# Kernel tuning notes

Hardware: AMD Instinct MI355X
Metric: run time of the kernel (lower is better)

Reference implementation:

```python
import jax, jax.numpy as jnp
import numpy as np

K_F = 3          # propagation kernel
PAD_F = 1
NUM = K_F * K_F - 1   # 8 non-reference neighbors
IDX_REF = NUM // 2    # 4
PROP_TIME = 18
B, H, W = 4, 240, 1216


def _conv2d_same(x, w, b):
    # x: (B,Cin,H,W), w: (Cout,Cin,kh,kw)
    y = jax.lax.conv_general_dilated(x, w, (1, 1), 'SAME',
                                     dimension_numbers=('NCHW', 'OIHW', 'NCHW'))
    return y + b[None, :, None, None]


def _bilinear(img, y, x):
    # img: (B,H,W); y,x: (B,K,H,W) float sample coords. Zero outside bounds (DCN semantics).
    Bv, Hv, Wv = img.shape
    flat = img.reshape(Bv, -1)
    y0 = jnp.floor(y)
    x0 = jnp.floor(x)
    wy = y - y0
    wx = x - x0

    def g(yy, xx):
        valid = (yy >= 0) & (yy <= Hv - 1) & (xx >= 0) & (xx <= Wv - 1)
        yc = jnp.clip(yy, 0, Hv - 1).astype(jnp.int32)
        xc = jnp.clip(xx, 0, Wv - 1).astype(jnp.int32)
        idx = (yc * Wv + xc).reshape(Bv, -1)
        v = jnp.take_along_axis(flat, idx, axis=1).reshape(yy.shape)
        return jnp.where(valid, v, jnp.zeros((), img.dtype))

    return ((1 - wy) * (1 - wx) * g(y0, x0)
            + (1 - wy) * wx * g(y0, x0 + 1)
            + wy * (1 - wx) * g(y1 := y0 + 1, x0)
            + wy * wx * g(y1, x0 + 1))


def _deform_agg(feat, off, mask, k, pad):
    # Modulated deformable conv with w == 1, b == 0, ch_f == 1.
    # feat: (B,1,H,W); off: (B,K,2,H,W) (dy,dx); mask: (B,K,H,W)
    Bv, _, Hv, Wv = feat.shape
    kk = jnp.arange(k)
    by = (jnp.repeat(kk, k) - pad).astype(feat.dtype)  # kernel base dy, row-major
    bx = (jnp.tile(kk, k) - pad).astype(feat.dtype)    # kernel base dx
    gy = jnp.arange(Hv, dtype=feat.dtype)[None, None, :, None]
    gx = jnp.arange(Wv, dtype=feat.dtype)[None, None, None, :]
    y = gy + by[None, :, None, None] + off[:, :, 0]
    x = gx + bx[None, :, None, None] + off[:, :, 1]
    s = _bilinear(feat[:, 0], y, x)                    # (B,K,H,W)
    return jnp.sum(s * mask, axis=1, keepdims=True)


def setup_inputs() -> dict:
    key = jax.random.key(0)
    k1, k2, k3, k4, k5, k6 = jax.random.split(key, 6)
    feat_init = jax.random.uniform(k1, (B, 1, H, W), jnp.float32)
    guidance = jax.random.normal(k2, (B, 8, H, W), jnp.float32)
    confidence = jax.random.uniform(k3, (B, 1, H, W), jnp.float32)
    dep = jax.random.uniform(k4, (B, 1, H, W), jnp.float32)
    valid = (jax.random.uniform(k5, (B, 1, H, W), jnp.float32) < 0.05)
    feat_fix = dep * valid.astype(jnp.float32)
    w_oa = 0.1 * jax.random.normal(k6, (3 * NUM, 8, 3, 3), jnp.float32)
    b_oa = jnp.zeros((3 * NUM,), jnp.float32)
    aff_scale_const = jnp.full((1,), 0.5 * NUM, jnp.float32)  # gamma * num (TGASS)
    return {'feat_init': feat_init, 'guidance': guidance, 'confidence': confidence,
            'feat_fix': feat_fix, 'w_oa': w_oa, 'b_oa': b_oa,
            'aff_scale_const': aff_scale_const}


def reference(feat_init, guidance, confidence, feat_fix, w_oa, b_oa, aff_scale_const):
    Bv, _, Hv, Wv = guidance.shape
    oa = _conv2d_same(guidance, w_oa, b_oa)                 # (B,24,H,W)
    o1, o2, aff = oa[:, :NUM], oa[:, NUM:2 * NUM], oa[:, 2 * NUM:]
    # torch: cat((o1,o2),1).view(B,num,2,H,W) then insert zero ref offset at idx_ref
    off = jnp.concatenate([o1, o2], axis=1).reshape(Bv, NUM, 2, Hv, Wv)
    zeros = jnp.zeros((Bv, 1, 2, Hv, Wv), off.dtype)
    off = jnp.concatenate([off[:, :IDX_REF], zeros, off[:, IDX_REF:]], axis=1)  # (B,9,2,H,W)

    # TGASS affinity
    aff = jnp.tanh(aff) / (aff_scale_const + 1e-8)          # (B,8,H,W)

    # confidence-weighted affinity: 1x1 deform-sample of confidence at each neighbor offset
    nbr = jnp.array([0, 1, 2, 3, 5, 6, 7, 8])
    off_c = jax.lax.stop_gradient(off[:, nbr])              # (B,8,2,H,W), offsets detached
    gy = jnp.arange(Hv, dtype=aff.dtype)[None, None, :, None]
    gx = jnp.arange(Wv, dtype=aff.dtype)[None, None, None, :]
    conf_aff = _bilinear(confidence[:, 0], gy + off_c[:, :, 0], gx + off_c[:, :, 1])
    aff = aff * conf_aff

    s = jnp.sum(jnp.abs(aff), axis=1, keepdims=True) + 1e-4
    s = jnp.maximum(s, 1.0)                                 # TGASS clamp
    aff = aff / s
    aff_ref = 1.0 - jnp.sum(aff, axis=1, keepdims=True)
    aff9 = jnp.concatenate([aff[:, :IDX_REF], aff_ref, aff[:, IDX_REF:]], axis=1)  # (B,9,H,W)

    # preserve_input mask
    mask_fix = (jnp.sum((feat_fix > 0.0).astype(feat_fix.dtype), axis=1, keepdims=True) > 0.0)
    mask_fix = jax.lax.stop_gradient(mask_fix.astype(feat_fix.dtype))

    def step(feat, _):
        feat = (1.0 - mask_fix) * feat + mask_fix * feat_fix
        feat = _deform_agg(feat, off, aff9, K_F, PAD_F)
        return feat, None

    feat_result, _ = jax.lax.scan(step, feat_init, None, length=PROP_TIME)
    return feat_result, off.reshape(Bv, -1, Hv, Wv), aff9
```

## Files before the change

### kernel.cpp

```cpp
#include <hip/hip_runtime.h>
#include <hip/hip_bf16.h>

#define B_ 4
#define H_ 240
#define W_ 1216
#define HW_ (H_*W_)
#define N1_ (B_*HW_)
#define PT_ 18

#define TROWS 11
#define TCOLS 274

__device__ __forceinline__ bool probe_bf16(const void* scale_ptr) {
    return ((const unsigned short*)scale_ptr)[0] == 0x4080;
}

__device__ __forceinline__ float ldin(const void* p, int i, bool bf) {
    if (bf) {
        unsigned int u = (unsigned int)((const unsigned short*)p)[i];
        return __uint_as_float(u << 16);
    }
    return ((const float*)p)[i];
}

__device__ __forceinline__ void stout(void* p, int i, bool bf, float v) {
    if (bf) ((__hip_bfloat16*)p)[i] = __float2bfloat16(v);
    else    ((float*)p)[i] = v;
}

__global__ __launch_bounds__(256) void k_prep_w(const void* __restrict__ w_oa,
                                                const void* __restrict__ b_oa,
                                                const void* __restrict__ scale,
                                                float* __restrict__ wc) {
    bool bf = probe_bf16(scale);
    int i = blockIdx.x * 256 + threadIdx.x;
    if (i < 1728) wc[i] = ldin(w_oa, i, bf);
    if (i < 24)   wc[1728 + i] = ldin(b_oa, i, bf);
}

__global__ __launch_bounds__(256) void k_init(const void* __restrict__ finit,
                                              const void* __restrict__ ffix,
                                              const void* __restrict__ scale,
                                              float* __restrict__ featA) {
    bool bf = probe_bf16(scale);
    int p = blockIdx.x * 256 + threadIdx.x;
    if (p >= N1_) return;
    float fx = ldin(ffix, p, bf);
    featA[p] = (fx > 0.0f) ? fx : ldin(finit, p, bf);
}

__global__ __launch_bounds__(256) void k_conv(const void* __restrict__ guid,
                                              const void* __restrict__ conf,
                                              const void* __restrict__ scale,
                                              const float* __restrict__ wc,
                                              void* __restrict__ d_out,
                                              float* __restrict__ ws_off,
                                              float* __restrict__ ws_aff,
                                              int mode2) {
    bool bf = probe_bf16(scale);
    int p = blockIdx.x * 256 + threadIdx.x;
    if (p >= N1_) return;
    int b = p / HW_;
    int r = p - b * HW_;
    int h = r / W_;
    int w = r - h * W_;

    float g[8][9];
    #pragma unroll
    for (int t = 0; t < 9; ++t) {
        int hh = h + t / 3 - 1;
        int ww = w + t % 3 - 1;
        bool v = (hh >= 0) && (hh < H_) && (ww >= 0) && (ww < W_);
        int idx0 = hh * W_ + ww;
        #pragma unroll
        for (int ci = 0; ci < 8; ++ci)
            g[ci][t] = v ? ldin(guid, (b * 8 + ci) * HW_ + idx0, bf) : 0.0f;
    }

    float oa[24];
    #pragma unroll
    for (int co = 0; co < 24; ++co) {
        float a = wc[1728 + co];
        #pragma unroll
        for (int ci = 0; ci < 8; ++ci)
            #pragma unroll
            for (int t = 0; t < 9; ++t)
                a = fmaf(g[ci][t], wc[(co * 8 + ci) * 9 + t], a);
        oa[co] = a;
    }

    float scl = ldin(scale, 0, bf);
    float inv = 1.0f / (scl + 1e-8f);

    float aft[8];
    int cbase = b * HW_;
    #pragma unroll
    for (int t = 0; t < 8; ++t) {
        float a = tanhf(oa[16 + t]) * inv;
        float y = (float)h + oa[2 * t];
        float x = (float)w + oa[2 * t + 1];
        float y0f = floorf(y), x0f = floorf(x);
        int y0 = (int)y0f, x0 = (int)x0f;
        float wy = y - y0f, wx = x - x0f;
        int y0c = min(max(y0, 0), H_ - 1), y1c = min(max(y0 + 1, 0), H_ - 1);
        int x0c = min(max(x0, 0), W_ - 1), x1c = min(max(x0 + 1, 0), W_ - 1);
        bool vy0 = (y0 >= 0) && (y0 < H_), vy1 = (y0 >= -1) && (y0 < H_ - 1);
        bool vx0 = (x0 >= 0) && (x0 < W_), vx1 = (x0 >= -1) && (x0 < W_ - 1);
        float w00 = (1.0f - wy) * (1.0f - wx); w00 = (vy0 && vx0) ? w00 : 0.0f;
        float w01 = (1.0f - wy) * wx;          w01 = (vy0 && vx1) ? w01 : 0.0f;
        float w10 = wy * (1.0f - wx);          w10 = (vy1 && vx0) ? w10 : 0.0f;
        float w11 = wy * wx;                   w11 = (vy1 && vx1) ? w11 : 0.0f;
        float f00 = ldin(conf, cbase + y0c * W_ + x0c, bf);
        float f01 = ldin(conf, cbase + y0c * W_ + x1c, bf);
        float f10 = ldin(conf, cbase + y1c * W_ + x0c, bf);
        float f11 = ldin(conf, cbase + y1c * W_ + x1c, bf);
        float cv = w00 * f00 + w01 * f01 + w10 * f10 + w11 * f11;
        aft[t] = a * cv;
    }
    float s = 1e-4f;
    #pragma unroll
    for (int t = 0; t < 8; ++t) s += fabsf(aft[t]);
    s = fmaxf(s, 1.0f);
    float rs = 1.0f / s;
    float suma = 0.0f;
    #pragma unroll
    for (int t = 0; t < 8; ++t) { aft[t] *= rs; suma += aft[t]; }
    float aref = 1.0f - suma;

    #pragma unroll
    for (int t = 0; t < 8; ++t) {
        int n9 = t + (t >= 4 ? 1 : 0);
        stout(d_out, N1_ + (b * 18 + 2 * n9)     * HW_ + r, bf, oa[2 * t]);
        stout(d_out, N1_ + (b * 18 + 2 * n9 + 1) * HW_ + r, bf, oa[2 * t + 1]);
        stout(d_out, 19 * N1_ + (b * 9 + n9) * HW_ + r, bf, aft[t]);
    }
    stout(d_out, N1_ + (b * 18 + 8) * HW_ + r, bf, 0.0f);
    stout(d_out, N1_ + (b * 18 + 9) * HW_ + r, bf, 0.0f);
    stout(d_out, 19 * N1_ + (b * 9 + 4) * HW_ + r, bf, aref);

    if (mode2) {
        #pragma unroll
        for (int t = 0; t < 8; ++t) {
            ws_off[t * N1_ + p]       = oa[2 * t];
            ws_off[(8 + t) * N1_ + p] = oa[2 * t + 1];
            int n9 = t + (t >= 4 ? 1 : 0);
            ws_aff[n9 * N1_ + p] = aft[t];
        }
        ws_aff[4 * N1_ + p] = aref;
    }
}

__global__ __launch_bounds__(256) void k_prop(const float* __restrict__ src,
                                              float* __restrict__ dst,
                                              const float* __restrict__ ws_off,
                                              const float* __restrict__ ws_aff,
                                              const void* __restrict__ d_out_all,
                                              const void* __restrict__ ffix_in,
                                              const void* __restrict__ scale,
                                              void* __restrict__ d_out_feat,
                                              int last, int mode2) {
    __shared__ float tile[TROWS][TCOLS];

    int tx = threadIdx.x;
    int bx = blockIdx.x;
    int h  = blockIdx.y;
    int b  = blockIdx.z;
    int w  = bx * 256 + tx;
    bool active = (w < W_);

    const float* sp = src + b * HW_;
    int row0 = h - 5;
    int col0 = bx * 256 - 8;

    bool bf = probe_bf16(scale);
    int r = h * W_ + w;
    int p = b * HW_ + r;
    float oy[8], ox[8], af[9], fxv = 0.0f;
    if (active) {
        if (mode2) {
            #pragma unroll
            for (int t = 0; t < 8; ++t) {
                oy[t] = ws_off[t * N1_ + p];
                ox[t] = ws_off[(8 + t) * N1_ + p];
            }
            #pragma unroll
            for (int n = 0; n < 9; ++n) af[n] = ws_aff[n * N1_ + p];
        } else {
            #pragma unroll
            for (int t = 0; t < 8; ++t) {
                int n9 = t + (t >= 4 ? 1 : 0);
                oy[t] = ldin(d_out_all, N1_ + (b * 18 + 2 * n9)     * HW_ + r, bf);
                ox[t] = ldin(d_out_all, N1_ + (b * 18 + 2 * n9 + 1) * HW_ + r, bf);
            }
            #pragma unroll
            for (int n = 0; n < 9; ++n)
                af[n] = ldin(d_out_all, 19 * N1_ + (b * 9 + n) * HW_ + r, bf);
        }
        if (!last) fxv = ldin(ffix_in, p, bf);
    }

    for (int idx = tx; idx < TROWS * TCOLS; idx += 256) {
        int rr = idx / TCOLS;
        int cc = idx - rr * TCOLS;
        int gy = min(max(row0 + rr, 0), H_ - 1);
        int gx = min(max(col0 + cc, 0), W_ - 1);
        tile[rr][cc] = sp[gy * W_ + gx];
    }
    __syncthreads();
    if (!active) return;

    float acc = af[4] * tile[5][tx + 8];

    #pragma unroll
    for (int t = 0; t < 8; ++t) {
        int n9 = t + (t >= 4 ? 1 : 0);
        float y = (float)(h + n9 / 3 - 1) + oy[t];
        float x = (float)(w + n9 % 3 - 1) + ox[t];
        float y0f = floorf(y), x0f = floorf(x);
        int y0 = (int)y0f, x0 = (int)x0f;
        float wy = y - y0f, wx = x - x0f;
        int y0c = min(max(y0, 0), H_ - 1), y1c = min(max(y0 + 1, 0), H_ - 1);
        int x0c = min(max(x0, 0), W_ - 1), x1c = min(max(x0 + 1, 0), W_ - 1);
        bool vy0 = (y0 >= 0) && (y0 < H_), vy1 = (y0 >= -1) && (y0 < H_ - 1);
        bool vx0 = (x0 >= 0) && (x0 < W_), vx1 = (x0 >= -1) && (x0 < W_ - 1);
        float w00 = (1.0f - wy) * (1.0f - wx); w00 = (vy0 && vx0) ? w00 : 0.0f;
        float w01 = (1.0f - wy) * wx;          w01 = (vy0 && vx1) ? w01 : 0.0f;
        float w10 = wy * (1.0f - wx);          w10 = (vy1 && vx0) ? w10 : 0.0f;
        float w11 = wy * wx;                   w11 = (vy1 && vx1) ? w11 : 0.0f;

        int sy0 = y0c - row0, sy1 = y1c - row0;
        int sx0 = x0c - col0, sx1 = x1c - col0;
        float f00, f01, f10, f11;
        if ((sy0 >= 0) && (sy1 <= TROWS - 1) && (sx0 >= 0) && (sx1 <= TCOLS - 1)) {
            f00 = tile[sy0][sx0];
            f01 = tile[sy0][sx1];
            f10 = tile[sy1][sx0];
            f11 = tile[sy1][sx1];
        } else {
            f00 = sp[y0c * W_ + x0c];
            f01 = sp[y0c * W_ + x1c];
            f10 = sp[y1c * W_ + x0c];
            f11 = sp[y1c * W_ + x1c];
        }
        float v = w00 * f00 + w01 * f01 + w10 * f10 + w11 * f11;
        acc = fmaf(af[n9], v, acc);
    }

    if (last) {
        stout(d_out_feat, p, bf, acc);
    } else {
        dst[p] = (fxv > 0.0f) ? fxv : acc;
    }
}

extern "C" void kernel_launch(void* const* d_in, const int* in_sizes, int n_in,
                              void* d_out, int out_size, void* d_ws, size_t ws_size,
                              hipStream_t stream) {
    const void* feat_init  = d_in[0];
    const void* guidance   = d_in[1];
    const void* confidence = d_in[2];
    const void* feat_fix   = d_in[3];
    const void* w_oa       = d_in[4];
    const void* b_oa       = d_in[5];
    const void* scale      = d_in[6];

    float* wsf    = (float*)d_ws;
    float* featA  = wsf;
    float* featB  = wsf + N1_;
    float* wc     = wsf + 2 * (size_t)N1_;
    float* ws_off = wsf + 2 * (size_t)N1_ + 2048;
    float* ws_aff = ws_off + 16 * (size_t)N1_;

    int is_bf16 = (in_sizes[4] < 1728 * 4) ? 1 : 0;
    size_t need2 = ((size_t)27 * N1_ + 2048) * sizeof(float);
    int mode2 = (is_bf16 && ws_size >= need2) ? 1 : 0;

    int grid = (N1_ + 255) / 256;
    hipLaunchKernelGGL(k_prep_w, dim3(7), dim3(256), 0, stream, w_oa, b_oa, scale, wc);
    hipLaunchKernelGGL(k_init, dim3(grid), dim3(256), 0, stream,
                       feat_init, feat_fix, scale, featA);
    hipLaunchKernelGGL(k_conv, dim3(grid), dim3(256), 0, stream,
                       guidance, confidence, scale, wc, d_out, ws_off, ws_aff, mode2);

    float* a = featA;
    float* bbuf = featB;
    dim3 pgrid(5, H_, B_);
    for (int it = 0; it < PT_; ++it) {
        int last = (it == PT_ - 1) ? 1 : 0;
        hipLaunchKernelGGL(k_prop, pgrid, dim3(256), 0, stream,
                           a, bbuf, ws_off, ws_aff, d_out, feat_fix, scale,
                           d_out, last, mode2);
        float* t = a; a = bbuf; bbuf = t;
    }
}
```

Before: 1.088 ms.

## Tile conv inputs in shared memory and process multiple rows per prop block

The conv kernel now runs on a 2D row-tiled grid. It stages the 3-row guidance window and a confidence tile in LDS, and reads transposed weights so each guidance value is broadcast across all 24 output channels. The propagation kernel handles four rows per block, which shares one taller feature tile and cuts halo reloads and launch block count. The mode2 gating is moved from a host check to a device-side bf16 probe. The trade-offs are more LDS per block and possibly lower occupancy.

Measured after the change: 1.711 ms. 1.57x slower.

```diff
diff --git a/kernel.cpp b/kernel.cpp
--- a/kernel.cpp
+++ b/kernel.cpp
@@ -11,6 +11,12 @@
 #define TROWS 11
 #define TCOLS 274
 
+#define PR_ 4
+#define TROWS2 (PR_ + 10)
+
+#define GCOLS 258
+#define GPITCH 260
+
 __device__ __forceinline__ bool probe_bf16(const void* scale_ptr) {
     return ((const unsigned short*)scale_ptr)[0] == 0x4080;
 }
@@ -34,8 +40,14 @@
                                                 float* __restrict__ wc) {
     bool bf = probe_bf16(scale);
     int i = blockIdx.x * 256 + threadIdx.x;
-    if (i < 1728) wc[i] = ldin(w_oa, i, bf);
-    if (i < 24)   wc[1728 + i] = ldin(b_oa, i, bf);
+    if (i < 1728) {
+        float v = ldin(w_oa, i, bf);
+        wc[i] = v;
+        int co = i / 72;
+        int rem = i - co * 72;
+        wc[1752 + rem * 24 + co] = v;
+    }
+    if (i < 24) wc[1728 + i] = ldin(b_oa, i, bf);
 }
 
 __global__ __launch_bounds__(256) void k_init(const void* __restrict__ finit,
@@ -57,43 +69,65 @@
                                               float* __restrict__ ws_off,
                                               float* __restrict__ ws_aff,
                                               int mode2) {
+    __shared__ float gt[8][3][GPITCH];
+    __shared__ float ct[TROWS][TCOLS];
+
+    int tx = threadIdx.x;
+    int bx = blockIdx.x;
+    int h  = blockIdx.y;
+    int b  = blockIdx.z;
+    int w  = bx * 256 + tx;
+    bool active = (w < W_);
     bool bf = probe_bf16(scale);
-    int p = blockIdx.x * 256 + threadIdx.x;
-    if (p >= N1_) return;
-    int b = p / HW_;
-    int r = p - b * HW_;
-    int h = r / W_;
-    int w = r - h * W_;
-
-    float g[8][9];
-    #pragma unroll
-    for (int t = 0; t < 9; ++t) {
-        int hh = h + t / 3 - 1;
-        int ww = w + t % 3 - 1;
-        bool v = (hh >= 0) && (hh < H_) && (ww >= 0) && (ww < W_);
-        int idx0 = hh * W_ + ww;
+
+    int col0g = bx * 256 - 1;
+    for (int idx = tx; idx < 8 * 3 * GCOLS; idx += 256) {
+        int ci = idx / (3 * GCOLS);
+        int rem = idx - ci * (3 * GCOLS);
+        int rr = rem / GCOLS;
+        int cc = rem - rr * GCOLS;
+        int gy = h - 1 + rr;
+        int gx = col0g + cc;
+        bool v = (gy >= 0) && (gy < H_) && (gx >= 0) && (gx < W_);
+        gt[ci][rr][cc] = v ? ldin(guid, (b * 8 + ci) * HW_ + gy * W_ + gx, bf) : 0.0f;
+    }
+    int row0 = h - 5;
+    int col0 = bx * 256 - 8;
+    int cbase = b * HW_;
+    for (int idx = tx; idx < TROWS * TCOLS; idx += 256) {
+        int rr = idx / TCOLS;
+        int cc = idx - rr * TCOLS;
+        int gy = min(max(row0 + rr, 0), H_ - 1);
+        int gx = min(max(col0 + cc, 0), W_ - 1);
+        ct[rr][cc] = ldin(conf, cbase + gy * W_ + gx, bf);
+    }
+    __syncthreads();
+    if (!active) return;
+
+    int r = h * W_ + w;
+    int p = cbase + r;
+
+    float oa[24];
+    #pragma unroll
+    for (int co = 0; co < 24; ++co) oa[co] = wc[1728 + co];
+
+    const float* wt = wc + 1752;
+    #pragma unroll
+    for (int ci = 0; ci < 8; ++ci) {
         #pragma unroll
-        for (int ci = 0; ci < 8; ++ci)
-            g[ci][t] = v ? ldin(guid, (b * 8 + ci) * HW_ + idx0, bf) : 0.0f;
-    }
-
-    float oa[24];
-    #pragma unroll
-    for (int co = 0; co < 24; ++co) {
-        float a = wc[1728 + co];
-        #pragma unroll
-        for (int ci = 0; ci < 8; ++ci)
-            #pragma unroll
-            for (int t = 0; t < 9; ++t)
-                a = fmaf(g[ci][t], wc[(co * 8 + ci) * 9 + t], a);
-        oa[co] = a;
+        for (int t = 0; t < 9; ++t) {
+            float gv = gt[ci][t / 3][tx + t % 3];
+            const float* wrow = wt + (ci * 9 + t) * 24;
+            #pragma unroll
+            for (int co = 0; co < 24; ++co)
+                oa[co] = fmaf(gv, wrow[co], oa[co]);
+        }
     }
 
     float scl = ldin(scale, 0, bf);
     float inv = 1.0f / (scl + 1e-8f);
 
     float aft[8];
-    int cbase = b * HW_;
     #pragma unroll
     for (int t = 0; t < 8; ++t) {
         float a = tanhf(oa[16 + t]) * inv;
@@ -110,10 +144,20 @@
         float w01 = (1.0f - wy) * wx;          w01 = (vy0 && vx1) ? w01 : 0.0f;
         float w10 = wy * (1.0f - wx);          w10 = (vy1 && vx0) ? w10 : 0.0f;
         float w11 = wy * wx;                   w11 = (vy1 && vx1) ? w11 : 0.0f;
-        float f00 = ldin(conf, cbase + y0c * W_ + x0c, bf);
-        float f01 = ldin(conf, cbase + y0c * W_ + x1c, bf);
-        float f10 = ldin(conf, cbase + y1c * W_ + x0c, bf);
-        float f11 = ldin(conf, cbase + y1c * W_ + x1c, bf);
+        int sy0 = y0c - row0, sy1 = y1c - row0;
+        int sx0 = x0c - col0, sx1 = x1c - col0;
+        float f00, f01, f10, f11;
+        if ((sy0 >= 0) && (sy1 <= TROWS - 1) && (sx0 >= 0) && (sx1 <= TCOLS - 1)) {
+            f00 = ct[sy0][sx0];
+            f01 = ct[sy0][sx1];
+            f10 = ct[sy1][sx0];
+            f11 = ct[sy1][sx1];
+        } else {
+            f00 = ldin(conf, cbase + y0c * W_ + x0c, bf);
+            f01 = ldin(conf, cbase + y0c * W_ + x1c, bf);
+            f10 = ldin(conf, cbase + y1c * W_ + x0c, bf);
+            f11 = ldin(conf, cbase + y1c * W_ + x1c, bf);
+        }
         float cv = w00 * f00 + w01 * f01 + w10 * f10 + w11 * f11;
         aft[t] = a * cv;
     }
@@ -138,7 +182,7 @@
     stout(d_out, N1_ + (b * 18 + 9) * HW_ + r, bf, 0.0f);
     stout(d_out, 19 * N1_ + (b * 9 + 4) * HW_ + r, bf, aref);
 
-    if (mode2) {
+    if (mode2 && bf) {
         #pragma unroll
         for (int t = 0; t < 8; ++t) {
             ws_off[t * N1_ + p]       = oa[2 * t];
@@ -159,25 +203,38 @@
                                               const void* __restrict__ scale,
                                               void* __restrict__ d_out_feat,
                                               int last, int mode2) {
-    __shared__ float tile[TROWS][TCOLS];
+    __shared__ float tile[TROWS2][TCOLS];
 
     int tx = threadIdx.x;
     int bx = blockIdx.x;
-    int h  = blockIdx.y;
+    int h0 = blockIdx.y * PR_;
     int b  = blockIdx.z;
     int w  = bx * 256 + tx;
     bool active = (w < W_);
+    bool bf = probe_bf16(scale);
+    bool use_ws = (mode2 != 0) && bf;
 
     const float* sp = src + b * HW_;
-    int row0 = h - 5;
+    int row0 = h0 - 5;
     int col0 = bx * 256 - 8;
 
-    bool bf = probe_bf16(scale);
-    int r = h * W_ + w;
-    int p = b * HW_ + r;
-    float oy[8], ox[8], af[9], fxv = 0.0f;
-    if (active) {
-        if (mode2) {
+    for (int idx = tx; idx < TROWS2 * TCOLS; idx += 256) {
+        int rr = idx / TCOLS;
+        int cc = idx - rr * TCOLS;
+        int gy = min(max(row0 + rr, 0), H_ - 1);
+        int gx = min(max(col0 + cc, 0), W_ - 1);
+        tile[rr][cc] = sp[gy * W_ + gx];
+    }
+    __syncthreads();
+    if (!active) return;
+
+    for (int ry = 0; ry < PR_; ++ry) {
+        int h = h0 + ry;
+        int r = h * W_ + w;
+        int p = b * HW_ + r;
+
+        float oy[8], ox[8], af[9];
+        if (use_ws) {
             #pragma unroll
             for (int t = 0; t < 8; ++t) {
                 oy[t] = ws_off[t * N1_ + p];
@@ -196,60 +253,50 @@
             for (int n = 0; n < 9; ++n)
                 af[n] = ldin(d_out_all, 19 * N1_ + (b * 9 + n) * HW_ + r, bf);
         }
-        if (!last) fxv = ldin(ffix_in, p, bf);
-    }
-
-    for (int idx = tx; idx < TROWS * TCOLS; idx += 256) {
-        int rr = idx / TCOLS;
-        int cc = idx - rr * TCOLS;
-        int gy = min(max(row0 + rr, 0), H_ - 1);
-        int gx = min(max(col0 + cc, 0), W_ - 1);
-        tile[rr][cc] = sp[gy * W_ + gx];
-    }
-    __syncthreads();
-    if (!active) return;
-
-    float acc = af[4] * tile[5][tx + 8];
-
-    #pragma unroll
-    for (int t = 0; t < 8; ++t) {
-        int n9 = t + (t >= 4 ? 1 : 0);
-        float y = (float)(h + n9 / 3 - 1) + oy[t];
-        float x = (float)(w + n9 % 3 - 1) + ox[t];
-        float y0f = floorf(y), x0f = floorf(x);
-        int y0 = (int)y0f, x0 = (int)x0f;
-        float wy = y - y0f, wx = x - x0f;
-        int y0c = min(max(y0, 0), H_ - 1), y1c = min(max(y0 + 1, 0), H_ - 1);
-        int x0c = min(max(x0, 0), W_ - 1), x1c = min(max(x0 + 1, 0), W_ - 1);
-        bool vy0 = (y0 >= 0) && (y0 < H_), vy1 = (y0 >= -1) && (y0 < H_ - 1);
-        bool vx0 = (x0 >= 0) && (x0 < W_), vx1 = (x0 >= -1) && (x0 < W_ - 1);
-        float w00 = (1.0f - wy) * (1.0f - wx); w00 = (vy0 && vx0) ? w00 : 0.0f;
-        float w01 = (1.0f - wy) * wx;          w01 = (vy0 && vx1) ? w01 : 0.0f;
-        float w10 = wy * (1.0f - wx);          w10 = (vy1 && vx0) ? w10 : 0.0f;
-        float w11 = wy * wx;                   w11 = (vy1 && vx1) ? w11 : 0.0f;
-
-        int sy0 = y0c - row0, sy1 = y1c - row0;
-        int sx0 = x0c - col0, sx1 = x1c - col0;
-        float f00, f01, f10, f11;
-        if ((sy0 >= 0) && (sy1 <= TROWS - 1) && (sx0 >= 0) && (sx1 <= TCOLS - 1)) {
-            f00 = tile[sy0][sx0];
-            f01 = tile[sy0][sx1];
-            f10 = tile[sy1][sx0];
-            f11 = tile[sy1][sx1];
+
+        float acc = af[4] * tile[5 + ry][tx + 8];
+
+        #pragma unroll
+        for (int t = 0; t < 8; ++t) {
+            int n9 = t + (t >= 4 ? 1 : 0);
+            float y = (float)(h + n9 / 3 - 1) + oy[t];
+            float x = (float)(w + n9 % 3 - 1) + ox[t];
+            float y0f = floorf(y), x0f = floorf(x);
+            int y0 = (int)y0f, x0 = (int)x0f;
+            float wy = y - y0f, wx = x - x0f;
+            int y0c = min(max(y0, 0), H_ - 1), y1c = min(max(y0 + 1, 0), H_ - 1);
+            int x0c = min(max(x0, 0), W_ - 1), x1c = min(max(x0 + 1, 0), W_ - 1);
+            bool vy0 = (y0 >= 0) && (y0 < H_), vy1 = (y0 >= -1) && (y0 < H_ - 1);
+            bool vx0 = (x0 >= 0) && (x0 < W_), vx1 = (x0 >= -1) && (x0 < W_ - 1);
+            float w00 = (1.0f - wy) * (1.0f - wx); w00 = (vy0 && vx0) ? w00 : 0.0f;
+            float w01 = (1.0f - wy) * wx;          w01 = (vy0 && vx1) ? w01 : 0.0f;
+            float w10 = wy * (1.0f - wx);          w10 = (vy1 && vx0) ? w10 : 0.0f;
+            float w11 = wy * wx;                   w11 = (vy1 && vx1) ? w11 : 0.0f;
+
+            int sy0 = y0c - row0, sy1 = y1c - row0;
+            int sx0 = x0c - col0, sx1 = x1c - col0;
+            float f00, f01, f10, f11;
+            if ((sy0 >= 0) && (sy1 <= TROWS2 - 1) && (sx0 >= 0) && (sx1 <= TCOLS - 1)) {
+                f00 = tile[sy0][sx0];
+                f01 = tile[sy0][sx1];
+                f10 = tile[sy1][sx0];
+                f11 = tile[sy1][sx1];
+            } else {
+                f00 = sp[y0c * W_ + x0c];
+                f01 = sp[y0c * W_ + x1c];
+                f10 = sp[y1c * W_ + x0c];
+                f11 = sp[y1c * W_ + x1c];
+            }
+            float v = w00 * f00 + w01 * f01 + w10 * f10 + w11 * f11;
+            acc = fmaf(af[n9], v, acc);
+        }
+
+        if (last) {
+            stout(d_out_feat, p, bf, acc);
         } else {
-            f00 = sp[y0c * W_ + x0c];
-            f01 = sp[y0c * W_ + x1c];
-            f10 = sp[y1c * W_ + x0c];
-            f11 = sp[y1c * W_ + x1c];
-        }
-        float v = w00 * f00 + w01 * f01 + w10 * f10 + w11 * f11;
-        acc = fmaf(af[n9], v, acc);
-    }
-
-    if (last) {
-        stout(d_out_feat, p, bf, acc);
-    } else {
-        dst[p] = (fxv > 0.0f) ? fxv : acc;
+            float fxv = ldin(ffix_in, p, bf);
+            dst[p] = (fxv > 0.0f) ? fxv : acc;
+        }
     }
 }
 
@@ -268,23 +315,22 @@
     float* featA  = wsf;
     float* featB  = wsf + N1_;
     float* wc     = wsf + 2 * (size_t)N1_;
-    float* ws_off = wsf + 2 * (size_t)N1_ + 2048;
+    float* ws_off = wsf + 2 * (size_t)N1_ + 4096;
     float* ws_aff = ws_off + 16 * (size_t)N1_;
 
-    int is_bf16 = (in_sizes[4] < 1728 * 4) ? 1 : 0;
-    size_t need2 = ((size_t)27 * N1_ + 2048) * sizeof(float);
-    int mode2 = (is_bf16 && ws_size >= need2) ? 1 : 0;
+    size_t need2 = ((size_t)27 * N1_ + 4096) * sizeof(float);
+    int mode2 = (ws_size >= need2) ? 1 : 0;
 
     int grid = (N1_ + 255) / 256;
     hipLaunchKernelGGL(k_prep_w, dim3(7), dim3(256), 0, stream, w_oa, b_oa, scale, wc);
     hipLaunchKernelGGL(k_init, dim3(grid), dim3(256), 0, stream,
                        feat_init, feat_fix, scale, featA);
-    hipLaunchKernelGGL(k_conv, dim3(grid), dim3(256), 0, stream,
+    hipLaunchKernelGGL(k_conv, dim3(5, H_, B_), dim3(256), 0, stream,
                        guidance, confidence, scale, wc, d_out, ws_off, ws_aff, mode2);
 
     float* a = featA;
     float* bbuf = featB;
-    dim3 pgrid(5, H_, B_);
+    dim3 pgrid(5, H_ / PR_, B_);
     for (int it = 0; it < PT_; ++it) {
         int last = (it == PT_ - 1) ? 1 : 0;
         hipLaunchKernelGGL(k_prop, pgrid, dim3(256), 0, stream,
```

## Process four output rows per propagation block to share the halo tile

Applied to the files above, without the earlier changes.

Each k_prop block now handles 4 consecutive rows, loading a 14-row shared tile once instead of an 11-row tile per single row. This cuts redundant halo loads from global memory by about 3x and quarters the block count. The cost is fewer blocks and so less parallelism, plus a serial row loop per thread. Separately, the decision to use the precomputed workspace is now made on the device from the bf16 probe rather than from host input sizes, and the workspace offset is shifted to make room.

New measurement: 990.5 us. 8.9% less time.

```diff
diff --git a/kernel.cpp b/kernel.cpp
--- a/kernel.cpp
+++ b/kernel.cpp
@@ -8,7 +8,8 @@
 #define N1_ (B_*HW_)
 #define PT_ 18
 
-#define TROWS 11
+#define PR_ 4
+#define TROWS2 (PR_ + 10)
 #define TCOLS 274
 
 __device__ __forceinline__ bool probe_bf16(const void* scale_ptr) {
@@ -138,7 +139,7 @@
     stout(d_out, N1_ + (b * 18 + 9) * HW_ + r, bf, 0.0f);
     stout(d_out, 19 * N1_ + (b * 9 + 4) * HW_ + r, bf, aref);
 
-    if (mode2) {
+    if (mode2 && bf) {
         #pragma unroll
         for (int t = 0; t < 8; ++t) {
             ws_off[t * N1_ + p]       = oa[2 * t];
@@ -159,25 +160,38 @@
                                               const void* __restrict__ scale,
                                               void* __restrict__ d_out_feat,
                                               int last, int mode2) {
-    __shared__ float tile[TROWS][TCOLS];
+    __shared__ float tile[TROWS2][TCOLS];
 
     int tx = threadIdx.x;
     int bx = blockIdx.x;
-    int h  = blockIdx.y;
+    int h0 = blockIdx.y * PR_;
     int b  = blockIdx.z;
     int w  = bx * 256 + tx;
     bool active = (w < W_);
+    bool bf = probe_bf16(scale);
+    bool use_ws = (mode2 != 0) && bf;
 
     const float* sp = src + b * HW_;
-    int row0 = h - 5;
+    int row0 = h0 - 5;
     int col0 = bx * 256 - 8;
 
-    bool bf = probe_bf16(scale);
-    int r = h * W_ + w;
-    int p = b * HW_ + r;
-    float oy[8], ox[8], af[9], fxv = 0.0f;
-    if (active) {
-        if (mode2) {
+    for (int idx = tx; idx < TROWS2 * TCOLS; idx += 256) {
+        int rr = idx / TCOLS;
+        int cc = idx - rr * TCOLS;
+        int gy = min(max(row0 + rr, 0), H_ - 1);
+        int gx = min(max(col0 + cc, 0), W_ - 1);
+        tile[rr][cc] = sp[gy * W_ + gx];
+    }
+    __syncthreads();
+    if (!active) return;
+
+    for (int ry = 0; ry < PR_; ++ry) {
+        int h = h0 + ry;
+        int r = h * W_ + w;
+        int p = b * HW_ + r;
+
+        float oy[8], ox[8], af[9];
+        if (use_ws) {
             #pragma unroll
             for (int t = 0; t < 8; ++t) {
                 oy[t] = ws_off[t * N1_ + p];
@@ -196,60 +210,50 @@
             for (int n = 0; n < 9; ++n)
                 af[n] = ldin(d_out_all, 19 * N1_ + (b * 9 + n) * HW_ + r, bf);
         }
-        if (!last) fxv = ldin(ffix_in, p, bf);
-    }
-
-    for (int idx = tx; idx < TROWS * TCOLS; idx += 256) {
-        int rr = idx / TCOLS;
-        int cc = idx - rr * TCOLS;
-        int gy = min(max(row0 + rr, 0), H_ - 1);
-        int gx = min(max(col0 + cc, 0), W_ - 1);
-        tile[rr][cc] = sp[gy * W_ + gx];
-    }
-    __syncthreads();
-    if (!active) return;
-
-    float acc = af[4] * tile[5][tx + 8];
-
-    #pragma unroll
-    for (int t = 0; t < 8; ++t) {
-        int n9 = t + (t >= 4 ? 1 : 0);
-        float y = (float)(h + n9 / 3 - 1) + oy[t];
-        float x = (float)(w + n9 % 3 - 1) + ox[t];
-        float y0f = floorf(y), x0f = floorf(x);
-        int y0 = (int)y0f, x0 = (int)x0f;
-        float wy = y - y0f, wx = x - x0f;
-        int y0c = min(max(y0, 0), H_ - 1), y1c = min(max(y0 + 1, 0), H_ - 1);
-        int x0c = min(max(x0, 0), W_ - 1), x1c = min(max(x0 + 1, 0), W_ - 1);
-        bool vy0 = (y0 >= 0) && (y0 < H_), vy1 = (y0 >= -1) && (y0 < H_ - 1);
-        bool vx0 = (x0 >= 0) && (x0 < W_), vx1 = (x0 >= -1) && (x0 < W_ - 1);
-        float w00 = (1.0f - wy) * (1.0f - wx); w00 = (vy0 && vx0) ? w00 : 0.0f;
-        float w01 = (1.0f - wy) * wx;          w01 = (vy0 && vx1) ? w01 : 0.0f;
-        float w10 = wy * (1.0f - wx);          w10 = (vy1 && vx0) ? w10 : 0.0f;
-        float w11 = wy * wx;                   w11 = (vy1 && vx1) ? w11 : 0.0f;
-
-        int sy0 = y0c - row0, sy1 = y1c - row0;
-        int sx0 = x0c - col0, sx1 = x1c - col0;
-        float f00, f01, f10, f11;
-        if ((sy0 >= 0) && (sy1 <= TROWS - 1) && (sx0 >= 0) && (sx1 <= TCOLS - 1)) {
-            f00 = tile[sy0][sx0];
-            f01 = tile[sy0][sx1];
-            f10 = tile[sy1][sx0];
-            f11 = tile[sy1][sx1];
+
+        float acc = af[4] * tile[5 + ry][tx + 8];
+
+        #pragma unroll
+        for (int t = 0; t < 8; ++t) {
+            int n9 = t + (t >= 4 ? 1 : 0);
+            float y = (float)(h + n9 / 3 - 1) + oy[t];
+            float x = (float)(w + n9 % 3 - 1) + ox[t];
+            float y0f = floorf(y), x0f = floorf(x);
+            int y0 = (int)y0f, x0 = (int)x0f;
+            float wy = y - y0f, wx = x - x0f;
+            int y0c = min(max(y0, 0), H_ - 1), y1c = min(max(y0 + 1, 0), H_ - 1);
+            int x0c = min(max(x0, 0), W_ - 1), x1c = min(max(x0 + 1, 0), W_ - 1);
+            bool vy0 = (y0 >= 0) && (y0 < H_), vy1 = (y0 >= -1) && (y0 < H_ - 1);
+            bool vx0 = (x0 >= 0) && (x0 < W_), vx1 = (x0 >= -1) && (x0 < W_ - 1);
+            float w00 = (1.0f - wy) * (1.0f - wx); w00 = (vy0 && vx0) ? w00 : 0.0f;
+            float w01 = (1.0f - wy) * wx;          w01 = (vy0 && vx1) ? w01 : 0.0f;
+            float w10 = wy * (1.0f - wx);          w10 = (vy1 && vx0) ? w10 : 0.0f;
+            float w11 = wy * wx;                   w11 = (vy1 && vx1) ? w11 : 0.0f;
+
+            int sy0 = y0c - row0, sy1 = y1c - row0;
+            int sx0 = x0c - col0, sx1 = x1c - col0;
+            float f00, f01, f10, f11;
+            if ((sy0 >= 0) && (sy1 <= TROWS2 - 1) && (sx0 >= 0) && (sx1 <= TCOLS - 1)) {
+                f00 = tile[sy0][sx0];
+                f01 = tile[sy0][sx1];
+                f10 = tile[sy1][sx0];
+                f11 = tile[sy1][sx1];
+            } else {
+                f00 = sp[y0c * W_ + x0c];
+                f01 = sp[y0c * W_ + x1c];
+                f10 = sp[y1c * W_ + x0c];
+                f11 = sp[y1c * W_ + x1c];
+            }
+            float v = w00 * f00 + w01 * f01 + w10 * f10 + w11 * f11;
+            acc = fmaf(af[n9], v, acc);
+        }
+
+        if (last) {
+            stout(d_out_feat, p, bf, acc);
         } else {
-            f00 = sp[y0c * W_ + x0c];
-            f01 = sp[y0c * W_ + x1c];
-            f10 = sp[y1c * W_ + x0c];
-            f11 = sp[y1c * W_ + x1c];
-        }
-        float v = w00 * f00 + w01 * f01 + w10 * f10 + w11 * f11;
-        acc = fmaf(af[n9], v, acc);
-    }
-
-    if (last) {
-        stout(d_out_feat, p, bf, acc);
-    } else {
-        dst[p] = (fxv > 0.0f) ? fxv : acc;
+            float fxv = ldin(ffix_in, p, bf);
+            dst[p] = (fxv > 0.0f) ? fxv : acc;
+        }
     }
 }
 
@@ -268,12 +272,11 @@
     float* featA  = wsf;
     float* featB  = wsf + N1_;
     float* wc     = wsf + 2 * (size_t)N1_;
-    float* ws_off = wsf + 2 * (size_t)N1_ + 2048;
+    float* ws_off = wsf + 2 * (size_t)N1_ + 4096;
     float* ws_aff = ws_off + 16 * (size_t)N1_;
 
-    int is_bf16 = (in_sizes[4] < 1728 * 4) ? 1 : 0;
-    size_t need2 = ((size_t)27 * N1_ + 2048) * sizeof(float);
-    int mode2 = (is_bf16 && ws_size >= need2) ? 1 : 0;
+    size_t need2 = ((size_t)27 * N1_ + 4096) * sizeof(float);
+    int mode2 = (ws_size >= need2) ? 1 : 0;
 
     int grid = (N1_ + 255) / 256;
     hipLaunchKernelGGL(k_prep_w, dim3(7), dim3(256), 0, stream, w_oa, b_oa, scale, wc);
@@ -284,7 +287,7 @@
 
     float* a = featA;
     float* bbuf = featB;
-    dim3 pgrid(5, H_, B_);
+    dim3 pgrid(5, H_ / PR_, B_);
     for (int it = 0; it < PT_; ++it) {
         int last = (it == PT_ - 1) ? 1 : 0;
         hipLaunchKernelGGL(k_prop, pgrid, dim3(256), 0, stream,
```
